# Performance work log

Hardware: AMD Instinct MI355X
Metric: run time of the kernel (lower is better)

Reference implementation:

```python
import jax, jax.numpy as jnp
import numpy as np

N_NODES = 50000
N_EDGES = 1600000
IN_DIM = 512
OUT_DIM = 256


def setup_inputs() -> dict:
    key = jax.random.key(0)
    k1, k2, k3, k4, k5, k6 = jax.random.split(key, 6)
    inputs = jax.random.normal(k1, (N_NODES, IN_DIM), dtype=jnp.float32)
    edge_row = jax.random.randint(k2, (N_EDGES,), 0, N_NODES, dtype=jnp.int32)
    edge_col = jax.random.randint(k3, (N_EDGES,), 0, N_NODES, dtype=jnp.int32)
    edge_val = jax.random.uniform(k4, (N_EDGES,), dtype=jnp.float32)
    stdv = 1.0 / np.sqrt(OUT_DIM)
    weight = jax.random.uniform(k5, (IN_DIM, OUT_DIM), dtype=jnp.float32, minval=-stdv, maxval=stdv)
    bias = jax.random.uniform(k6, (OUT_DIM,), dtype=jnp.float32, minval=-stdv, maxval=stdv)
    return {"inputs": inputs, "edge_row": edge_row, "edge_col": edge_col,
            "edge_val": edge_val, "weight": weight, "bias": bias}


def reference(inputs, edge_row, edge_col, edge_val, weight, bias):
    # dense GEMM: [N, in] @ [in, out] -> [N, out]
    support = inputs @ weight
    # SpMM: out[r] += val * support[c] for each edge (r, c, val)
    gathered = edge_val[:, None] * support[edge_col]  # [E, out]
    output = jax.ops.segment_sum(gathered, edge_row, num_segments=N_NODES)
    return output + bias
```

## Files before the change

### kernel.cpp

```cpp
#include <hip/hip_runtime.h>

#define N_NODES 50000
#define N_EDGES 1600000
#define IN_DIM 512
#define OUT_DIM 256

#define BM 64
#define BN 256
#define BK 32
#define APAD 8
#define LDA (BK + APAD)

#define RPB   128
#define NBKT  391
#define CHUNK 4096
#define EPT   16
#define CAP   5120

typedef unsigned int u32;
typedef unsigned short u16;
typedef short bf16x8 __attribute__((ext_vector_type(8)));
typedef float f32x4 __attribute__((ext_vector_type(4)));

__device__ __forceinline__ float bf_to_f(u16 u) { return __uint_as_float(((u32)u) << 16); }
__device__ __forceinline__ u16 f_to_bf(float f) {
    u32 u = __float_as_uint(f);
    u32 r = (u + 0x7fffu + ((u >> 16) & 1u)) >> 16;
    return (u16)r;
}

__global__ __launch_bounds__(256) void scatter1(const int* __restrict__ er,
                                                const int* __restrict__ ec,
                                                const float* __restrict__ ev,
                                                int* __restrict__ cursor,
                                                int2* __restrict__ tmp) {
    __shared__ int  hcnt[NBKT];
    __shared__ int  loff[NBKT];
    __shared__ int  gbase[NBKT];
    __shared__ int  sc[512];
    __shared__ int2 estage[CHUNK];
    __shared__ u16  bslot[CHUNK];

    const int t = threadIdx.x;
    const int base = blockIdx.x * CHUNK;
    const int nedge = min(CHUNK, N_EDGES - base);

    for (int k = t; k < NBKT; k += 256) hcnt[k] = 0;
    __syncthreads();

    int w0[EPT], w1[EPT], rk[EPT];
    #pragma unroll
    for (int j = 0; j < EPT; ++j) {
        const int i = j * 256 + t;
        rk[j] = -1;
        if (i < nedge) {
            const int e = base + i;
            const int r = er[e];
            const int bk = r >> 7;
            w0[j] = ec[e] | ((r & 127) << 16) | (bk << 23);
            w1[j] = __float_as_int(ev[e]);
            rk[j] = atomicAdd(&hcnt[bk], 1);
        }
    }
    __syncthreads();

    sc[t]       = (t < NBKT) ? hcnt[t] : 0;
    sc[t + 256] = (t + 256 < NBKT) ? hcnt[t + 256] : 0;
    __syncthreads();
    #pragma unroll
    for (int off = 1; off < 512; off <<= 1) {
        const int a0 = (t >= off) ? sc[t - off] : 0;
        const int a1 = sc[t + 256 - off];
        __syncthreads();
        sc[t] += a0;
        sc[t + 256] += a1;
        __syncthreads();
    }
    if (t < NBKT)       loff[t]       = sc[t] - hcnt[t];
    if (t + 256 < NBKT) loff[t + 256] = sc[t + 256] - hcnt[t + 256];

    if (t < NBKT && hcnt[t] > 0)
        gbase[t] = t * CAP + atomicAdd(&cursor[t], hcnt[t]);
    if (t + 256 < NBKT && hcnt[t + 256] > 0)
        gbase[t + 256] = (t + 256) * CAP + atomicAdd(&cursor[t + 256], hcnt[t + 256]);
    __syncthreads();

    #pragma unroll
    for (int j = 0; j < EPT; ++j) {
        if (rk[j] >= 0) {
            const int bk = ((u32)w0[j]) >> 23;
            const int s = loff[bk] + rk[j];
            estage[s] = make_int2(w0[j], w1[j]);
            bslot[s]  = (u16)bk;
        }
    }
    __syncthreads();

    for (int s = t; s < nedge; s += 256) {
        const int bk = bslot[s];
        const int2 e2 = estage[s];
        const int gpos = gbase[bk] + (s - loff[bk]);
        if (gpos < (bk + 1) * CAP)
            tmp[gpos] = e2;
    }
}

__global__ __launch_bounds__(256) void wcvt_zero(const float* __restrict__ W,
                                                 u16* __restrict__ WT,
                                                 int* __restrict__ cursor) {
    if (blockIdx.x < 2) {
        const int i = blockIdx.x * 256 + threadIdx.x;
        if (i < NBKT) cursor[i] = 0;
    }
    const int n  = threadIdx.x;
    const int k0 = blockIdx.x * 4;
    ushort4 o;
    o.x = f_to_bf(W[(size_t)(k0 + 0) * OUT_DIM + n]);
    o.y = f_to_bf(W[(size_t)(k0 + 1) * OUT_DIM + n]);
    o.z = f_to_bf(W[(size_t)(k0 + 2) * OUT_DIM + n]);
    o.w = f_to_bf(W[(size_t)(k0 + 3) * OUT_DIM + n]);
    *(ushort4*)(WT + (size_t)n * IN_DIM + k0) = o;
}

__global__ __launch_bounds__(256) void fused_s2_gemm(const int* __restrict__ cursor,
                                                     const int2* __restrict__ tmp,
                                                     int* __restrict__ row_ptr,
                                                     int2* __restrict__ sedge,
                                                     const float* __restrict__ X,
                                                     const u16* __restrict__ WT,
                                                     u16* __restrict__ Sb) {
    __shared__ __align__(16) char smem[BM * LDA * 2 + BN * LDA * 2];

    const int t = threadIdx.x;

    if (blockIdx.x < NBKT) {
        int* sc   = (int*)smem;
        int* orig = sc + 512;
        int* rcnt = orig + 512;
        int* rsc  = rcnt + RPB;
        int* rcur = rsc + RPB;
        const int b = blockIdx.x;

        const int c0 = (t < NBKT) ? min(cursor[t], CAP) : 0;
        const int c1 = (t + 256 < NBKT) ? min(cursor[t + 256], CAP) : 0;
        sc[t] = c0;       orig[t] = c0;
        sc[t + 256] = c1; orig[t + 256] = c1;
        __syncthreads();
        #pragma unroll
        for (int off = 1; off < 512; off <<= 1) {
            const int a0 = (t >= off) ? sc[t - off] : 0;
            const int a1 = sc[t + 256 - off];
            __syncthreads();
            sc[t] += a0;
            sc[t + 256] += a1;
            __syncthreads();
        }
        const int gb = sc[b] - orig[b];
        const int n  = orig[b];
        const int2* src = tmp + (size_t)b * CAP;

        if (b == 0 && t == 0) row_ptr[N_NODES] = N_EDGES;

        if (t < RPB) rcnt[t] = 0;
        __syncthreads();
        for (int i = t; i < n; i += 256)
            atomicAdd(&rcnt[(((u32)src[i].x) >> 16) & 127], 1);
        __syncthreads();

        if (t < RPB) rsc[t] = rcnt[t];
        __syncthreads();
        #pragma unroll
        for (int off = 1; off < RPB; off <<= 1) {
            int a = 0;
            if (t < RPB && t >= off) a = rsc[t - off];
            __syncthreads();
            if (t < RPB) rsc[t] += a;
            __syncthreads();
        }
        if (t < RPB) {
            const int excl = rsc[t] - rcnt[t];
            rcur[t] = gb + excl;
            const int row = b * RPB + t;
            if (row < N_NODES) row_ptr[row] = gb + excl;
        }
        __syncthreads();

        for (int i = t; i < n; i += 256) {
            const int2 e2 = src[i];
            const int rloc = (((u32)e2.x) >> 16) & 127;
            const int pos = atomicAdd(&rcur[rloc], 1);
            sedge[pos] = make_int2(e2.x & 0xFFFF, e2.y);
        }
    } else {
        u16* As = (u16*)smem;
        u16* Bs = (u16*)(smem + BM * LDA * 2);

        const int wave = t >> 6;
        const int lane = t & 63;
        const int r0   = (blockIdx.x - NBKT) * BM;
        const int wn   = wave * 64;
        const int l15  = lane & 15;
        const int quad = lane >> 4;

        f32x4 acc[4][4];
        #pragma unroll
        for (int i = 0; i < 4; ++i)
            #pragma unroll
            for (int j = 0; j < 4; ++j) acc[i][j] = (f32x4)0.f;

        const int arow = t >> 2;
        const int akp  = (t & 3) * 8;
        const int xrow = min(r0 + arow, N_NODES - 1);
        const float* xsrc = X + (size_t)xrow * IN_DIM + akp;
        const int brow = t >> 1;
        const int bkp  = (t & 1) * 16;
        const u16* bsrc  = WT + (size_t)brow * IN_DIM + bkp;
        const u16* bsrc2 = bsrc + (size_t)128 * IN_DIM;

        float4 fA0 = *(const float4*)(xsrc + 0);
        float4 fA1 = *(const float4*)(xsrc + 4);
        uint4  rB0 = *(const uint4*)(bsrc + 0);
        uint4  rB1 = *(const uint4*)(bsrc + 8);
        uint4  rB2 = *(const uint4*)(bsrc2 + 0);
        uint4  rB3 = *(const uint4*)(bsrc2 + 8);

        for (int kc = 0; kc < IN_DIM; kc += BK) {
            {
                ushort4 p0, p1;
                p0.x = f_to_bf(fA0.x); p0.y = f_to_bf(fA0.y); p0.z = f_to_bf(fA0.z); p0.w = f_to_bf(fA0.w);
                p1.x = f_to_bf(fA1.x); p1.y = f_to_bf(fA1.y); p1.z = f_to_bf(fA1.z); p1.w = f_to_bf(fA1.w);
                *(ushort4*)&As[arow * LDA + akp + 0] = p0;
                *(ushort4*)&As[arow * LDA + akp + 4] = p1;
                *(uint4*)&Bs[brow * LDA + bkp + 0] = rB0;
                *(uint4*)&Bs[brow * LDA + bkp + 8] = rB1;
                *(uint4*)&Bs[(brow + 128) * LDA + bkp + 0] = rB2;
                *(uint4*)&Bs[(brow + 128) * LDA + bkp + 8] = rB3;
            }
            __syncthreads();

            if (kc + BK < IN_DIM) {
                fA0 = *(const float4*)(xsrc + kc + BK + 0);
                fA1 = *(const float4*)(xsrc + kc + BK + 4);
                rB0 = *(const uint4*)(bsrc + kc + BK + 0);
                rB1 = *(const uint4*)(bsrc + kc + BK + 8);
                rB2 = *(const uint4*)(bsrc2 + kc + BK + 0);
                rB3 = *(const uint4*)(bsrc2 + kc + BK + 8);
            }

            bf16x8 af[4], bfr[4];
            #pragma unroll
            for (int mt = 0; mt < 4; ++mt)
                af[mt] = *(const bf16x8*)&As[(mt * 16 + l15) * LDA + quad * 8];
            #pragma unroll
            for (int nt = 0; nt < 4; ++nt)
                bfr[nt] = *(const bf16x8*)&Bs[(wn + nt * 16 + l15) * LDA + quad * 8];
            #pragma unroll
            for (int mt = 0; mt < 4; ++mt)
                #pragma unroll
                for (int nt = 0; nt < 4; ++nt)
                    acc[mt][nt] = __builtin_amdgcn_mfma_f32_16x16x32_bf16(
                        af[mt], bfr[nt], acc[mt][nt], 0, 0, 0);
            __syncthreads();
        }

        #pragma unroll
        for (int mt = 0; mt < 4; ++mt) {
            #pragma unroll
            for (int r = 0; r < 4; ++r) {
                const int grow = r0 + mt * 16 + quad * 4 + r;
                if (grow < N_NODES) {
                    u16* dst = Sb + (size_t)grow * OUT_DIM + wn + l15;
                    #pragma unroll
                    for (int nt = 0; nt < 4; ++nt)
                        dst[nt * 16] = f_to_bf(acc[mt][nt][r]);
                }
            }
        }
    }
}

__global__ __launch_bounds__(256) void csr_spmm(const int* __restrict__ row_ptr,
                                                const int2* __restrict__ sedge,
                                                const u16* __restrict__ Sb,
                                                const float* __restrict__ bias,
                                                float* __restrict__ out,
                                                int rbase) {
    const int wave = threadIdx.x >> 6;
    const int lane = threadIdx.x & 63;
    const int r = rbase + blockIdx.x * 4 + wave;
    if (r >= N_NODES) return;

    const int start = row_ptr[r];
    const int end   = row_ptr[r + 1];

    float4 acc = *(const float4*)(bias + lane * 4);
    const u16* sbase = Sb + lane * 4;

    int e = start;
    for (; e + 16 <= end; e += 16) {
        int2 ed[16];
        #pragma unroll
        for (int j = 0; j < 16; ++j) ed[j] = sedge[e + j];

        ushort4 sv[16];
        #pragma unroll
        for (int j = 0; j < 16; ++j)
            sv[j] = *(const ushort4*)(sbase + (size_t)ed[j].x * OUT_DIM);

        #pragma unroll
        for (int j = 0; j < 16; ++j) {
            const float vj = __int_as_float(ed[j].y);
            acc.x += vj * bf_to_f(sv[j].x);
            acc.y += vj * bf_to_f(sv[j].y);
            acc.z += vj * bf_to_f(sv[j].z);
            acc.w += vj * bf_to_f(sv[j].w);
        }
    }
    if (e < end) {
        int2 ed[16];
        #pragma unroll
        for (int j = 0; j < 16; ++j)
            ed[j] = sedge[min(e + j, end - 1)];
        #pragma unroll
        for (int j = 0; j < 16; ++j)
            if (e + j >= end) ed[j].y = 0;

        ushort4 sv[16];
        #pragma unroll
        for (int j = 0; j < 16; ++j)
            sv[j] = *(const ushort4*)(sbase + (size_t)ed[j].x * OUT_DIM);

        #pragma unroll
        for (int j = 0; j < 16; ++j) {
            const float vj = __int_as_float(ed[j].y);
            acc.x += vj * bf_to_f(sv[j].x);
            acc.y += vj * bf_to_f(sv[j].y);
            acc.z += vj * bf_to_f(sv[j].z);
            acc.w += vj * bf_to_f(sv[j].w);
        }
    }

    *(float4*)(out + (size_t)r * OUT_DIM + lane * 4) = acc;
}

extern "C" void kernel_launch(void* const* d_in, const int* in_sizes, int n_in,
                              void* d_out, int out_size, void* d_ws, size_t ws_size,
                              hipStream_t stream) {
    const float* X    = (const float*)d_in[0];
    const int*   er   = (const int*)d_in[1];
    const int*   ec   = (const int*)d_in[2];
    const float* ev   = (const float*)d_in[3];
    const float* W    = (const float*)d_in[4];
    const float* bias = (const float*)d_in[5];
    float* out        = (float*)d_out;

    char* ws = (char*)d_ws;
    u16*  Sb      = (u16*) (ws);
    int2* sedge   = (int2*)(ws + 25600000);
    int2* tmp     = (int2*)(ws + 38400000);
    u16*  WT      = (u16*) (ws + 54415360);
    int*  row_ptr = (int*) (ws + 54677504);
    int*  cursor  = (int*) (ws + 54877508);

    hipLaunchKernelGGL(wcvt_zero, dim3(IN_DIM / 4), dim3(256), 0, stream,
                       W, WT, cursor);
    hipLaunchKernelGGL(scatter1, dim3((N_EDGES + CHUNK - 1) / CHUNK), dim3(256), 0,
                       stream, er, ec, ev, cursor, tmp);
    hipLaunchKernelGGL(fused_s2_gemm, dim3(NBKT + (N_NODES + BM - 1) / BM),
                       dim3(256), 0, stream,
                       cursor, tmp, row_ptr, sedge, X, WT, Sb);
    hipLaunchKernelGGL(csr_spmm, dim3(25000 / 4), dim3(256), 0, stream,
                       row_ptr, sedge, Sb, bias, out, 0);
    hipLaunchKernelGGL(csr_spmm, dim3(25000 / 4), dim3(256), 0, stream,
                       row_ptr, sedge, Sb, bias, out, 25000);
}
```

Measured before the change: 360.5 us.

## Fuse edge bucket scatter with GEMM and split second-stage scatter out

Moves the first edge-bucketing pass into the same launch as the dense GEMM, so bucketing overlaps the GEMM, and moves the per-row CSR construction into its own kernel. The two half-range SpMM launches become a single launch. This trades the old overlap of scatter stage 2 with the GEMM for overlap of stage 1, and raises the fused kernel's shared memory to about 47 KB, which may lower GEMM occupancy.

```diff
diff --git a/kernel.cpp b/kernel.cpp
--- a/kernel.cpp
+++ b/kernel.cpp
@@ -27,82 +27,6 @@
     u32 u = __float_as_uint(f);
     u32 r = (u + 0x7fffu + ((u >> 16) & 1u)) >> 16;
     return (u16)r;
-}
-
-__global__ __launch_bounds__(256) void scatter1(const int* __restrict__ er,
-                                                const int* __restrict__ ec,
-                                                const float* __restrict__ ev,
-                                                int* __restrict__ cursor,
-                                                int2* __restrict__ tmp) {
-    __shared__ int  hcnt[NBKT];
-    __shared__ int  loff[NBKT];
-    __shared__ int  gbase[NBKT];
-    __shared__ int  sc[512];
-    __shared__ int2 estage[CHUNK];
-    __shared__ u16  bslot[CHUNK];
-
-    const int t = threadIdx.x;
-    const int base = blockIdx.x * CHUNK;
-    const int nedge = min(CHUNK, N_EDGES - base);
-
-    for (int k = t; k < NBKT; k += 256) hcnt[k] = 0;
-    __syncthreads();
-
-    int w0[EPT], w1[EPT], rk[EPT];
-    #pragma unroll
-    for (int j = 0; j < EPT; ++j) {
-        const int i = j * 256 + t;
-        rk[j] = -1;
-        if (i < nedge) {
-            const int e = base + i;
-            const int r = er[e];
-            const int bk = r >> 7;
-            w0[j] = ec[e] | ((r & 127) << 16) | (bk << 23);
-            w1[j] = __float_as_int(ev[e]);
-            rk[j] = atomicAdd(&hcnt[bk], 1);
-        }
-    }
-    __syncthreads();
-
-    sc[t]       = (t < NBKT) ? hcnt[t] : 0;
-    sc[t + 256] = (t + 256 < NBKT) ? hcnt[t + 256] : 0;
-    __syncthreads();
-    #pragma unroll
-    for (int off = 1; off < 512; off <<= 1) {
-        const int a0 = (t >= off) ? sc[t - off] : 0;
-        const int a1 = sc[t + 256 - off];
-        __syncthreads();
-        sc[t] += a0;
-        sc[t + 256] += a1;
-        __syncthreads();
-    }
-    if (t < NBKT)       loff[t]       = sc[t] - hcnt[t];
-    if (t + 256 < NBKT) loff[t + 256] = sc[t + 256] - hcnt[t + 256];
-
-    if (t < NBKT && hcnt[t] > 0)
-        gbase[t] = t * CAP + atomicAdd(&cursor[t], hcnt[t]);
-    if (t + 256 < NBKT && hcnt[t + 256] > 0)
-        gbase[t + 256] = (t + 256) * CAP + atomicAdd(&cursor[t + 256], hcnt[t + 256]);
-    __syncthreads();
-
-    #pragma unroll
-    for (int j = 0; j < EPT; ++j) {
-        if (rk[j] >= 0) {
-            const int bk = ((u32)w0[j]) >> 23;
-            const int s = loff[bk] + rk[j];
-            estage[s] = make_int2(w0[j], w1[j]);
-            bslot[s]  = (u16)bk;
-        }
-    }
-    __syncthreads();
-
-    for (int s = t; s < nedge; s += 256) {
-        const int bk = bslot[s];
-        const int2 e2 = estage[s];
-        const int gpos = gbase[bk] + (s - loff[bk]);
-        if (gpos < (bk + 1) * CAP)
-            tmp[gpos] = e2;
-    }
 }
 
 __global__ __launch_bounds__(256) void wcvt_zero(const float* __restrict__ W,
@@ -122,29 +46,50 @@
     *(ushort4*)(WT + (size_t)n * IN_DIM + k0) = o;
 }
 
-__global__ __launch_bounds__(256) void fused_s2_gemm(const int* __restrict__ cursor,
-                                                     const int2* __restrict__ tmp,
-                                                     int* __restrict__ row_ptr,
-                                                     int2* __restrict__ sedge,
+__global__ __launch_bounds__(256) void fused_s1_gemm(const int* __restrict__ er,
+                                                     const int* __restrict__ ec,
+                                                     const float* __restrict__ ev,
+                                                     int* __restrict__ cursor,
+                                                     int2* __restrict__ tmp,
                                                      const float* __restrict__ X,
                                                      const u16* __restrict__ WT,
                                                      u16* __restrict__ Sb) {
-    __shared__ __align__(16) char smem[BM * LDA * 2 + BN * LDA * 2];
+    __shared__ __align__(16) char smem[47712];
 
     const int t = threadIdx.x;
 
     if (blockIdx.x < NBKT) {
-        int* sc   = (int*)smem;
-        int* orig = sc + 512;
-        int* rcnt = orig + 512;
-        int* rsc  = rcnt + RPB;
-        int* rcur = rsc + RPB;
-        const int b = blockIdx.x;
-
-        const int c0 = (t < NBKT) ? min(cursor[t], CAP) : 0;
-        const int c1 = (t + 256 < NBKT) ? min(cursor[t + 256], CAP) : 0;
-        sc[t] = c0;       orig[t] = c0;
-        sc[t + 256] = c1; orig[t + 256] = c1;
+        int2* estage = (int2*)smem;
+        u16*  bslot  = (u16*)(smem + 32768);
+        int*  hcnt   = (int*)(smem + 40960);
+        int*  loff   = (int*)(smem + 42524);
+        int*  gbase  = (int*)(smem + 44088);
+        int*  sc     = (int*)(smem + 45652);
+
+        const int base = blockIdx.x * CHUNK;
+        const int nedge = min(CHUNK, N_EDGES - base);
+
+        for (int k = t; k < NBKT; k += 256) hcnt[k] = 0;
+        __syncthreads();
+
+        int w0[EPT], w1[EPT], rk[EPT];
+        #pragma unroll
+        for (int j = 0; j < EPT; ++j) {
+            const int i = j * 256 + t;
+            rk[j] = -1;
+            if (i < nedge) {
+                const int e = base + i;
+                const int r = er[e];
+                const int bk = r >> 7;
+                w0[j] = ec[e] | ((r & 127) << 16) | (bk << 23);
+                w1[j] = __float_as_int(ev[e]);
+                rk[j] = atomicAdd(&hcnt[bk], 1);
+            }
+        }
+        __syncthreads();
+
+        sc[t]       = (t < NBKT) ? hcnt[t] : 0;
+        sc[t + 256] = (t + 256 < NBKT) ? hcnt[t + 256] : 0;
         __syncthreads();
         #pragma unroll
         for (int off = 1; off < 512; off <<= 1) {
@@ -155,41 +100,32 @@
             sc[t + 256] += a1;
             __syncthreads();
         }
-        const int gb = sc[b] - orig[b];
-        const int n  = orig[b];
-        const int2* src = tmp + (size_t)b * CAP;
-
-        if (b == 0 && t == 0) row_ptr[N_NODES] = N_EDGES;
-
-        if (t < RPB) rcnt[t] = 0;
-        __syncthreads();
-        for (int i = t; i < n; i += 256)
-            atomicAdd(&rcnt[(((u32)src[i].x) >> 16) & 127], 1);
-        __syncthreads();
-
-        if (t < RPB) rsc[t] = rcnt[t];
-        __syncthreads();
-        #pragma unroll
-        for (int off = 1; off < RPB; off <<= 1) {
-            int a = 0;
-            if (t < RPB && t >= off) a = rsc[t - off];
-            __syncthreads();
-            if (t < RPB) rsc[t] += a;
-            __syncthreads();
-        }
-        if (t < RPB) {
-            const int excl = rsc[t] - rcnt[t];
-            rcur[t] = gb + excl;
-            const int row = b * RPB + t;
-            if (row < N_NODES) row_ptr[row] = gb + excl;
-        }
-        __syncthreads();
-
-        for (int i = t; i < n; i += 256) {
-            const int2 e2 = src[i];
-            const int rloc = (((u32)e2.x) >> 16) & 127;
-            const int pos = atomicAdd(&rcur[rloc], 1);
-            sedge[pos] = make_int2(e2.x & 0xFFFF, e2.y);
+        if (t < NBKT)       loff[t]       = sc[t] - hcnt[t];
+        if (t + 256 < NBKT) loff[t + 256] = sc[t + 256] - hcnt[t + 256];
+
+        if (t < NBKT && hcnt[t] > 0)
+            gbase[t] = t * CAP + atomicAdd(&cursor[t], hcnt[t]);
+        if (t + 256 < NBKT && hcnt[t + 256] > 0)
+            gbase[t + 256] = (t + 256) * CAP + atomicAdd(&cursor[t + 256], hcnt[t + 256]);
+        __syncthreads();
+
+        #pragma unroll
+        for (int j = 0; j < EPT; ++j) {
+            if (rk[j] >= 0) {
+                const int bk = ((u32)w0[j]) >> 23;
+                const int s = loff[bk] + rk[j];
+                estage[s] = make_int2(w0[j], w1[j]);
+                bslot[s]  = (u16)bk;
+            }
+        }
+        __syncthreads();
+
+        for (int s = t; s < nedge; s += 256) {
+            const int bk = bslot[s];
+            const int2 e2 = estage[s];
+            const int gpos = gbase[bk] + (s - loff[bk]);
+            if (gpos < (bk + 1) * CAP)
+                tmp[gpos] = e2;
         }
     } else {
         u16* As = (u16*)smem;
@@ -279,15 +215,78 @@
     }
 }
 
+__global__ __launch_bounds__(256) void scatter2(const int* __restrict__ cursor,
+                                                const int2* __restrict__ tmp,
+                                                int* __restrict__ row_ptr,
+                                                int2* __restrict__ sedge) {
+    __shared__ int sc[512];
+    __shared__ int orig[512];
+    __shared__ int rcnt[RPB];
+    __shared__ int rsc[RPB];
+    __shared__ int rcur[RPB];
+    const int t = threadIdx.x;
+    const int b = blockIdx.x;
+
+    const int c0 = (t < NBKT) ? min(cursor[t], CAP) : 0;
+    const int c1 = (t + 256 < NBKT) ? min(cursor[t + 256], CAP) : 0;
+    sc[t] = c0;       orig[t] = c0;
+    sc[t + 256] = c1; orig[t + 256] = c1;
+    __syncthreads();
+    #pragma unroll
+    for (int off = 1; off < 512; off <<= 1) {
+        const int a0 = (t >= off) ? sc[t - off] : 0;
+        const int a1 = sc[t + 256 - off];
+        __syncthreads();
+        sc[t] += a0;
+        sc[t + 256] += a1;
+        __syncthreads();
+    }
+    const int gb = sc[b] - orig[b];
+    const int n  = orig[b];
+    const int2* src = tmp + (size_t)b * CAP;
+
+    if (b == 0 && t == 0) row_ptr[N_NODES] = N_EDGES;
+
+    if (t < RPB) rcnt[t] = 0;
+    __syncthreads();
+    for (int i = t; i < n; i += 256)
+        atomicAdd(&rcnt[(((u32)src[i].x) >> 16) & 127], 1);
+    __syncthreads();
+
+    if (t < RPB) rsc[t] = rcnt[t];
+    __syncthreads();
+    #pragma unroll
+    for (int off = 1; off < RPB; off <<= 1) {
+        int a = 0;
+        if (t < RPB && t >= off) a = rsc[t - off];
+        __syncthreads();
+        if (t < RPB) rsc[t] += a;
+        __syncthreads();
+    }
+    if (t < RPB) {
+        const int excl = rsc[t] - rcnt[t];
+        rcur[t] = gb + excl;
+        const int row = b * RPB + t;
+        if (row < N_NODES) row_ptr[row] = gb + excl;
+    }
+    __syncthreads();
+
+    for (int i = t; i < n; i += 256) {
+        const int2 e2 = src[i];
+        const int rloc = (((u32)e2.x) >> 16) & 127;
+        const int pos = atomicAdd(&rcur[rloc], 1);
+        sedge[pos] = make_int2(e2.x & 0xFFFF, e2.y);
+    }
+}
+
 __global__ __launch_bounds__(256) void csr_spmm(const int* __restrict__ row_ptr,
                                                 const int2* __restrict__ sedge,
                                                 const u16* __restrict__ Sb,
                                                 const float* __restrict__ bias,
-                                                float* __restrict__ out,
-                                                int rbase) {
+                                                float* __restrict__ out) {
     const int wave = threadIdx.x >> 6;
     const int lane = threadIdx.x & 63;
-    const int r = rbase + blockIdx.x * 4 + wave;
+    const int r = blockIdx.x * 4 + wave;
     if (r >= N_NODES) return;
 
     const int start = row_ptr[r];
@@ -364,13 +363,11 @@
 
     hipLaunchKernelGGL(wcvt_zero, dim3(IN_DIM / 4), dim3(256), 0, stream,
                        W, WT, cursor);
-    hipLaunchKernelGGL(scatter1, dim3((N_EDGES + CHUNK - 1) / CHUNK), dim3(256), 0,
-                       stream, er, ec, ev, cursor, tmp);
-    hipLaunchKernelGGL(fused_s2_gemm, dim3(NBKT + (N_NODES + BM - 1) / BM),
+    hipLaunchKernelGGL(fused_s1_gemm, dim3(NBKT + (N_NODES + BM - 1) / BM),
                        dim3(256), 0, stream,
-                       cursor, tmp, row_ptr, sedge, X, WT, Sb);
-    hipLaunchKernelGGL(csr_spmm, dim3(25000 / 4), dim3(256), 0, stream,
-                       row_ptr, sedge, Sb, bias, out, 0);
-    hipLaunchKernelGGL(csr_spmm, dim3(25000 / 4), dim3(256), 0, stream,
-                       row_ptr, sedge, Sb, bias, out, 25000);
-}
+                       er, ec, ev, cursor, tmp, X, WT, Sb);
+    hipLaunchKernelGGL(scatter2, dim3(NBKT), dim3(256), 0, stream,
+                       cursor, tmp, row_ptr, sedge);
+    hipLaunchKernelGGL(csr_spmm, dim3((N_NODES + 3) / 4), dim3(256), 0, stream,
+                       row_ptr, sedge, Sb, bias, out);
+}
```

Result: faster. 348.6 us (-3.3%).
